# Kernel tuning notes

Hardware: AMD Instinct MI355X
Metric: run time of the kernel (lower is better)

The kernel has to match this reference:

```python
import jax, jax.numpy as jnp
import numpy as np

N, E, F_IN, F_OUT = 50000, 1600000, 256, 64
ALPHA = 0.2  # LeakyReLU negative slope


def setup_inputs() -> dict:
    key = jax.random.key(0)
    k1, k2, k3, k4 = jax.random.split(key, 4)
    x = jax.random.normal(k1, (N, F_IN), dtype=jnp.float32)
    edge = jax.random.randint(k2, (2, E), 0, N)  # COO (row, col) indices of adj
    # xavier_normal with gain=1.414 (as in the torch module)
    W = jax.random.normal(k3, (F_IN, F_OUT), dtype=jnp.float32) * (1.414 * np.sqrt(2.0 / (F_IN + F_OUT)))
    a = jax.random.normal(k4, (1, 2 * F_OUT), dtype=jnp.float32) * (1.414 * np.sqrt(2.0 / (1 + 2 * F_OUT)))
    return {"x": x, "edge": edge, "W": W, "a": a}


def reference(x, edge, W, a):
    # eval mode: dropout is a no-op
    Wh = x @ W  # [N, F_OUT]
    src, dst = edge[0], edge[1]
    # a @ concat(Wh[src], Wh[dst]) per edge, computed as two node-level dots then gathered
    s_src = Wh @ a[0, :F_OUT]   # [N]
    s_dst = Wh @ a[0, F_OUT:]   # [N]
    score = s_src[src] + s_dst[dst]                      # [E]
    edge_e = jnp.exp(-jax.nn.leaky_relu(score, ALPHA))   # [E]
    # sparse-softmax denominator: row sums of exp scores
    e_rowsum = jax.ops.segment_sum(edge_e, src, num_segments=N)  # [N]
    # weighted aggregation: h_prime[i] = sum_{(i,j) in E} e_ij * Wh[j]
    h_prime = jax.ops.segment_sum(edge_e[:, None] * Wh[dst], src, num_segments=N)  # [N, F_OUT]
    h_prime = h_prime / e_rowsum[:, None]
    return jax.nn.elu(h_prime)  # concat=True -> ELU
```

## Files before the change

### kernel.cpp

```cpp
#include <hip/hip_runtime.h>
#include <hip/hip_fp16.h>

#define N_NODES 50000
#define N_EDGES 1600000
#define F_IN 256
#define F_OUT 64
#define ALPHA 0.2f

#define BS 64
#define NBK 782
#define NSUB 8
#define CAP 384
#define EB 4096
#define NBB 391
#define LDS_CAP 4096
#define OF_CAP 16384

typedef __attribute__((ext_vector_type(8))) short bf16x8;
typedef __attribute__((ext_vector_type(4))) float f32x4;

__device__ inline unsigned short f2bf(float f) {
    unsigned int u = __float_as_uint(f);
    return (unsigned short)((u + 0x7FFFu + ((u >> 16) & 1u)) >> 16);
}
__device__ inline float bf2f(unsigned short b) {
    return __uint_as_float(((unsigned int)b) << 16);
}

__device__ inline void fmix_lo(float& a, unsigned int u, float s) {
    asm("v_fma_mix_f32 %0, %1, %2, %0 op_sel:[0,0,0] op_sel_hi:[1,0,0]"
        : "+v"(a) : "v"(u), "v"(s));
}
__device__ inline void fmix_hi(float& a, unsigned int u, float s) {
    asm("v_fma_mix_f32 %0, %1, %2, %0 op_sel:[1,0,0] op_sel_hi:[1,0,0]"
        : "+v"(a) : "v"(u), "v"(s));
}

__global__ __launch_bounds__(256) void gat_wprep(
    const float* __restrict__ W, unsigned short* __restrict__ Wf,
    int* __restrict__ cnt, int* __restrict__ of_cnt)
{
    const int di = blockIdx.x * 256 + threadIdx.x;
    if (di < NSUB * NBK) cnt[di] = 0;
    if (di == 0) of_cnt[0] = 0;
    const int j    = di & 7;
    const int lane = (di >> 3) & 63;
    const int tile = di >> 9;
    const int ks   = tile >> 2;
    const int nt   = tile & 3;
    const int k = ks * 32 + (lane >> 4) * 8 + j;
    const int n = nt * 16 + (lane & 15);
    Wf[di] = f2bf(W[k * F_OUT + n]);
}

__global__ __launch_bounds__(256) void gat_fused(
    const float* __restrict__ x, const unsigned short* __restrict__ Wf,
    const float* __restrict__ a, unsigned short* __restrict__ Whh,
    float* __restrict__ s_src, float* __restrict__ s_dst,
    const int* __restrict__ edge, int* __restrict__ cnt,
    unsigned int* __restrict__ arr, int* __restrict__ of_cnt,
    int2* __restrict__ of_list)
{
    __shared__ __align__(16) unsigned char smem[32768];
    const int t = threadIdx.x;

    if (blockIdx.x < NBK) {
        unsigned short* Wl = (unsigned short*)smem;
        {
            const float4* __restrict__ src = (const float4*)Wf;
            float4* dst = (float4*)Wl;
            #pragma unroll
            for (int i = 0; i < 8; ++i) dst[t + i * 256] = src[t + i * 256];
        }
        __syncthreads();

        const int lane = t & 63;
        const int w    = t >> 6;
        const int q    = lane >> 4;
        const int c16  = lane & 15;
        const bf16x8* __restrict__ Wfrag = (const bf16x8*)Wl;

        float av[4], av2[4];
        #pragma unroll
        for (int nt = 0; nt < 4; ++nt) {
            av[nt]  = a[nt * 16 + c16];
            av2[nt] = a[F_OUT + nt * 16 + c16];
        }

        const int c = blockIdx.x;
        const int node0 = c * 64 + w * 16;
        int row = node0 + c16;
        if (row >= N_NODES) row = N_NODES - 1;
        const float4* __restrict__ xp = (const float4*)(x + (size_t)row * F_IN);

        float4 xv[16];
        #pragma unroll
        for (int ks = 0; ks < 8; ++ks) {
            xv[2 * ks]     = xp[ks * 8 + q * 2];
            xv[2 * ks + 1] = xp[ks * 8 + q * 2 + 1];
        }

        f32x4 acc[4];
        #pragma unroll
        for (int nt = 0; nt < 4; ++nt) acc[nt] = (f32x4){0.f, 0.f, 0.f, 0.f};

        #pragma unroll
        for (int ks = 0; ks < 8; ++ks) {
            float xf[8] = {xv[2*ks].x,   xv[2*ks].y,   xv[2*ks].z,   xv[2*ks].w,
                           xv[2*ks+1].x, xv[2*ks+1].y, xv[2*ks+1].z, xv[2*ks+1].w};
            bf16x8 ah, al;
            #pragma unroll
            for (int j = 0; j < 8; ++j) {
                const unsigned short h = f2bf(xf[j]);
                ah[j] = (short)h;
                al[j] = (short)f2bf(xf[j] - bf2f(h));
            }
            #pragma unroll
            for (int nt = 0; nt < 4; ++nt) {
                const bf16x8 bh = Wfrag[(ks * 4 + nt) * 64 + lane];
                acc[nt] = __builtin_amdgcn_mfma_f32_16x16x32_bf16(ah, bh, acc[nt], 0, 0, 0);
                acc[nt] = __builtin_amdgcn_mfma_f32_16x16x32_bf16(al, bh, acc[nt], 0, 0, 0);
            }
        }

        #pragma unroll
        for (int r = 0; r < 4; ++r) {
            const int node = node0 + q * 4 + r;
            float p = 0.f, qq = 0.f;
            #pragma unroll
            for (int nt = 0; nt < 4; ++nt) {
                const float v = acc[nt][r];
                if (node < N_NODES)
                    Whh[(size_t)node * F_OUT + nt * 16 + c16] =
                        __half_as_ushort(__float2half(v));
                p  = fmaf(v, av[nt], p);
                qq = fmaf(v, av2[nt], qq);
            }
            #pragma unroll
            for (int off = 1; off <= 8; off <<= 1) {
                p  += __shfl_xor(p, off);
                qq += __shfl_xor(qq, off);
            }
            if (c16 == 0 && node < N_NODES) { s_src[node] = p; s_dst[node] = qq; }
        }
    } else {
        int* lhist            = (int*)smem;
        int* lstart           = (int*)(smem + 3128);
        int* gbase            = (int*)(smem + 6260);
        int* cursor           = (int*)(smem + 9388);
        int* scanbuf          = (int*)(smem + 12516);
        unsigned int* sorted  = (unsigned int*)(smem + 13540);

        const int blk = blockIdx.x - NBK;
        const int e0  = blk * EB;
        const int sub = blk & 7;

        for (int i = t; i < NBK; i += 256) lhist[i] = 0;
        __syncthreads();

        int sreg[EB / 256];
        #pragma unroll
        for (int i = 0; i < EB / 256; ++i) {
            const int e = e0 + i * 256 + t;
            int s = -1;
            if (e < N_EDGES) {
                s = edge[e];
                atomicAdd(&lhist[s >> 6], 1);
            }
            sreg[i] = s;
        }
        __syncthreads();

        int psum = 0;
        {
            const int b0 = t * 4;
            #pragma unroll
            for (int i = 0; i < 4; ++i)
                if (b0 + i < NBK) psum += lhist[b0 + i];
        }
        scanbuf[t] = psum;
        __syncthreads();
        for (int off = 1; off < 256; off <<= 1) {
            const int v = (t >= off) ? scanbuf[t - off] : 0;
            __syncthreads();
            scanbuf[t] += v;
            __syncthreads();
        }
        {
            int run = scanbuf[t] - psum;
            const int b0 = t * 4;
            #pragma unroll
            for (int i = 0; i < 4; ++i) {
                const int b = b0 + i;
                if (b < NBK) {
                    lstart[b] = run;
                    cursor[b] = run;
                    run += lhist[b];
                }
            }
            if (t == 255) lstart[NBK] = scanbuf[255];
        }
        __syncthreads();

        for (int b = t; b < NBK; b += 256) {
            const int c = lhist[b];
            gbase[b] = (c > 0) ? atomicAdd(&cnt[sub * NBK + b], c) : 0;
        }

        #pragma unroll
        for (int i = 0; i < EB / 256; ++i) {
            const int s = sreg[i];
            if (s >= 0) {
                const int e = e0 + i * 256 + t;
                const int d = edge[N_EDGES + e];
                const int b = s >> 6;
                const int pos = atomicAdd(&cursor[b], 1);
                sorted[pos] = ((unsigned)b << 22) | ((unsigned)(s & 63) << 16) | (unsigned)d;
            }
        }
        __syncthreads();

        const int C = lstart[NBK];
        for (int p = t; p < C; p += 256) {
            const unsigned en = sorted[p];
            const int b = (int)(en >> 22);
            const int idx = gbase[b] + (p - lstart[b]);
            if (idx < CAP) {
                arr[((size_t)(sub * NBK + b)) * CAP + idx] = en & 0x3FFFFFu;
            } else {
                const int s = b * 64 + (int)((en >> 16) & 63);
                const int op = atomicAdd(of_cnt, 1);
                if (op < OF_CAP) of_list[op] = make_int2(s, (int)(en & 0xFFFFu));
            }
        }
    }
}

__global__ __launch_bounds__(512) void gat_aggregate(
    const int* __restrict__ cnt, const unsigned int* __restrict__ arr,
    const float* __restrict__ s_src, const float* __restrict__ s_dst,
    const unsigned short* __restrict__ Whh, const int* __restrict__ of_cnt,
    const int2* __restrict__ of_list, float* __restrict__ out)
{
    __shared__ uint2 ent2[LDS_CAP + 32];
    __shared__ int   bin[BS];
    __shared__ int   start[BS + 1];
    __shared__ int   Pl[NSUB + 1];
    const int t = threadIdx.x;
    const int lane = t & 63;
    const int w = t >> 6;
    const int b = blockIdx.x;

    if (t < BS) bin[t] = 0;
    if (t < 32) ent2[LDS_CAP + t] = make_uint2(0u, 0u);
    if (w == 0) {
        int c = (lane < NSUB) ? min(cnt[lane * NBK + b], CAP) : 0;
        int s = c;
        #pragma unroll
        for (int off = 1; off < NSUB; off <<= 1) {
            const int v = __shfl_up(s, off);
            if (lane >= off) s += v;
        }
        if (lane < NSUB) Pl[lane + 1] = s;
        if (lane == 0)   Pl[0] = 0;
    }
    __syncthreads();
    const int C = Pl[NSUB];
    const int nof = min(of_cnt[0], OF_CAP);

    unsigned enr[6];
    int nr = 0;
    for (int g = t; g < C; g += 512) {
        int sub = 0;
        #pragma unroll
        for (int s2 = 1; s2 < NSUB; ++s2) sub += (g >= Pl[s2]);
        const unsigned en = arr[((size_t)(sub * NBK + b)) * CAP + (g - Pl[sub])];
        enr[nr++] = en;
        atomicAdd(&bin[en >> 16], 1);
    }
    for (int i = t; i < nof; i += 512) {
        const int2 e2 = of_list[i];
        if ((e2.x >> 6) == b) atomicAdd(&bin[e2.x & 63], 1);
    }
    __syncthreads();
    if (w == 0) {
        const int c  = bin[lane];
        const int pc = (c + 31) & ~31;
        int s = pc;
        #pragma unroll
        for (int off = 1; off < BS; off <<= 1) {
            const int v = __shfl_up(s, off);
            if (lane >= off) s += v;
        }
        start[lane + 1] = s;
        if (lane == 0) start[0] = 0;
        bin[lane] = s - pc;
    }
    __syncthreads();

    for (int r = 0; r < nr; ++r) {
        const unsigned en = enr[r];
        const int sl = (int)(en >> 16);
        const int d  = (int)(en & 0xffffu);
        const float sc = s_src[b * BS + sl] + s_dst[d];
        const float ee = __expf(-(sc > 0.f ? sc : ALPHA * sc));
        const int pos = atomicAdd(&bin[sl], 1);
        if (pos < LDS_CAP) ent2[pos] = make_uint2((unsigned)d, __float_as_uint(ee));
    }
    for (int i = t; i < nof; i += 512) {
        const int2 e2 = of_list[i];
        if ((e2.x >> 6) == b) {
            const float sc = s_src[e2.x] + s_dst[e2.y];
            const float ee = __expf(-(sc > 0.f ? sc : ALPHA * sc));
            const int pos = atomicAdd(&bin[e2.x & 63], 1);
            if (pos < LDS_CAP) ent2[pos] = make_uint2((unsigned)e2.y, __float_as_uint(ee));
        }
    }
    __syncthreads();
    {
        const int n  = t & 63;
        const int e1 = min(start[n + 1], LDS_CAP);
        for (int p = bin[n] + (t >> 6); p < e1; p += 8)
            ent2[p] = make_uint2(0u, 0u);
    }
    __syncthreads();

    const int q  = lane >> 4;
    const int fq = lane & 15;
    const uint2* __restrict__ Whh2 = (const uint2*)Whh;

    for (int n = w * 8; n < w * 8 + 8; ++n) {
        const int node = b * BS + n;
        if (node >= N_NODES) break;
        const int r0 = start[n];
        const int r1 = min(start[n + 1], LDS_CAP);
        float4 acc = make_float4(0.f, 0.f, 0.f, 0.f);
        float rsum = 0.f;
        for (int j = r0; j < r1; j += 32) {
            unsigned eu[8];
            uint2 wv[8];
            #pragma unroll
            for (int k = 0; k < 8; ++k) {
                const uint2 e = ent2[j + 4 * k + q];
                eu[k] = e.y;
                wv[k] = Whh2[(size_t)e.x * 16 + fq];
            }
            #pragma unroll
            for (int k = 0; k < 8; ++k) {
                const float et = __uint_as_float(eu[k]);
                fmix_lo(acc.x, wv[k].x, et);
                fmix_hi(acc.y, wv[k].x, et);
                fmix_lo(acc.z, wv[k].y, et);
                fmix_hi(acc.w, wv[k].y, et);
                rsum += et;
            }
        }
        acc.x += __shfl_xor(acc.x, 16); acc.x += __shfl_xor(acc.x, 32);
        acc.y += __shfl_xor(acc.y, 16); acc.y += __shfl_xor(acc.y, 32);
        acc.z += __shfl_xor(acc.z, 16); acc.z += __shfl_xor(acc.z, 32);
        acc.w += __shfl_xor(acc.w, 16); acc.w += __shfl_xor(acc.w, 32);
        rsum  += __shfl_xor(rsum, 16);  rsum  += __shfl_xor(rsum, 32);

        const float rinv = __builtin_amdgcn_rcpf(rsum);
        float4 v;
        v.x = acc.x * rinv; v.y = acc.y * rinv;
        v.z = acc.z * rinv; v.w = acc.w * rinv;
        v.x = v.x > 0.f ? v.x : (__expf(v.x) - 1.f);
        v.y = v.y > 0.f ? v.y : (__expf(v.y) - 1.f);
        v.z = v.z > 0.f ? v.z : (__expf(v.z) - 1.f);
        v.w = v.w > 0.f ? v.w : (__expf(v.w) - 1.f);
        if (q == 0)
            ((float4*)out)[(size_t)node * 16 + fq] = v;
    }
}

extern "C" void kernel_launch(void* const* d_in, const int* in_sizes, int n_in,
                              void* d_out, int out_size, void* d_ws, size_t ws_size,
                              hipStream_t stream) {
    const float* x    = (const float*)d_in[0];
    const int*   edge = (const int*)  d_in[1];
    const float* W    = (const float*)d_in[2];
    const float* a    = (const float*)d_in[3];
    float* out = (float*)d_out;

    unsigned short* Whh   = (unsigned short*)d_ws;
    unsigned int*   arr   = (unsigned int*)(Whh + (size_t)N_NODES * F_OUT);
    float*          s_src = (float*)(arr + (size_t)NSUB * NBK * CAP);
    float*          s_dst = s_src + N_NODES;
    int*            cnt   = (int*)(s_dst + N_NODES);
    int2*           of_list = (int2*)(cnt + NSUB * NBK);
    int*            of_cnt  = (int*)(of_list + OF_CAP);
    unsigned short* Wf      = (unsigned short*)(of_cnt + 4);

    gat_wprep<<<64, 256, 0, stream>>>(W, Wf, cnt, of_cnt);
    gat_fused<<<NBK + NBB, 256, 0, stream>>>(x, Wf, a, Whh, s_src, s_dst,
                                             edge, cnt, arr, of_cnt, of_list);
    gat_aggregate<<<NBK, 512, 0, stream>>>(cnt, arr, s_src, s_dst, Whh,
                                           of_cnt, of_list, out);
}
```

Measured before the change: 154.7 us.

## Split aggregation into score and gather kernels with packed bf16 CSR

The aggregation kernel is split in two. A score kernel computes edge weights and writes a per-node CSR to global memory, packing the destination index and a bf16 weight into one 32-bit word. A separate gather kernel then assigns one wavefront per node across 6250 blocks, which gives more parallelism and load balance than the old 8 nodes per wave in LDS. The fused kernel's block order is also swapped so the edge-sorting blocks are scheduled first. The trade-offs are an extra global round trip and a kernel launch, plus bf16 rounding of the edge weights.

Result: slower. 159.7 us (+3.2%).

```diff
diff --git a/kernel.cpp b/kernel.cpp
--- a/kernel.cpp
+++ b/kernel.cpp
@@ -13,7 +13,7 @@
 #define CAP 384
 #define EB 4096
 #define NBB 391
-#define LDS_CAP 4096
+#define BCAP 4096
 #define OF_CAP 16384
 
 typedef __attribute__((ext_vector_type(8))) short bf16x8;
@@ -64,7 +64,7 @@
     __shared__ __align__(16) unsigned char smem[32768];
     const int t = threadIdx.x;
 
-    if (blockIdx.x < NBK) {
+    if (blockIdx.x >= NBB) {
         unsigned short* Wl = (unsigned short*)smem;
         {
             const float4* __restrict__ src = (const float4*)Wf;
@@ -87,7 +87,7 @@
             av2[nt] = a[F_OUT + nt * 16 + c16];
         }
 
-        const int c = blockIdx.x;
+        const int c = blockIdx.x - NBB;
         const int node0 = c * 64 + w * 16;
         int row = node0 + c16;
         if (row >= N_NODES) row = N_NODES - 1;
@@ -151,7 +151,7 @@
         int* scanbuf          = (int*)(smem + 12516);
         unsigned int* sorted  = (unsigned int*)(smem + 13540);
 
-        const int blk = blockIdx.x - NBK;
+        const int blk = blockIdx.x;
         const int e0  = blk * EB;
         const int sub = blk & 7;
 
@@ -236,23 +236,22 @@
     }
 }
 
-__global__ __launch_bounds__(512) void gat_aggregate(
+__global__ __launch_bounds__(512) void gat_score(
     const int* __restrict__ cnt, const unsigned int* __restrict__ arr,
     const float* __restrict__ s_src, const float* __restrict__ s_dst,
-    const unsigned short* __restrict__ Whh, const int* __restrict__ of_cnt,
-    const int2* __restrict__ of_list, float* __restrict__ out)
+    const int* __restrict__ of_cnt, const int2* __restrict__ of_list,
+    unsigned int* __restrict__ csr, int* __restrict__ abase,
+    int* __restrict__ pcnt)
 {
-    __shared__ uint2 ent2[LDS_CAP + 32];
-    __shared__ int   bin[BS];
-    __shared__ int   start[BS + 1];
-    __shared__ int   Pl[NSUB + 1];
+    __shared__ int bin[BS];
+    __shared__ int start[BS + 1];
+    __shared__ int Pl[NSUB + 1];
     const int t = threadIdx.x;
     const int lane = t & 63;
     const int w = t >> 6;
     const int b = blockIdx.x;
 
     if (t < BS) bin[t] = 0;
-    if (t < 32) ent2[LDS_CAP + t] = make_uint2(0u, 0u);
     if (w == 0) {
         int c = (lane < NSUB) ? min(cnt[lane * NBK + b], CAP) : 0;
         int s = c;
@@ -297,6 +296,8 @@
         bin[lane] = s - pc;
     }
     __syncthreads();
+
+    unsigned int* __restrict__ csrb = csr + (size_t)b * BCAP;
 
     for (int r = 0; r < nr; ++r) {
         const unsigned en = enr[r];
@@ -305,7 +306,7 @@
         const float sc = s_src[b * BS + sl] + s_dst[d];
         const float ee = __expf(-(sc > 0.f ? sc : ALPHA * sc));
         const int pos = atomicAdd(&bin[sl], 1);
-        if (pos < LDS_CAP) ent2[pos] = make_uint2((unsigned)d, __float_as_uint(ee));
+        if (pos < BCAP) csrb[pos] = ((unsigned)d << 16) | (unsigned)f2bf(ee);
     }
     for (int i = t; i < nof; i += 512) {
         const int2 e2 = of_list[i];
@@ -313,65 +314,75 @@
             const float sc = s_src[e2.x] + s_dst[e2.y];
             const float ee = __expf(-(sc > 0.f ? sc : ALPHA * sc));
             const int pos = atomicAdd(&bin[e2.x & 63], 1);
-            if (pos < LDS_CAP) ent2[pos] = make_uint2((unsigned)e2.y, __float_as_uint(ee));
+            if (pos < BCAP) csrb[pos] = ((unsigned)e2.y << 16) | (unsigned)f2bf(ee);
         }
     }
     __syncthreads();
     {
         const int n  = t & 63;
-        const int e1 = min(start[n + 1], LDS_CAP);
-        for (int p = bin[n] + (t >> 6); p < e1; p += 8)
-            ent2[p] = make_uint2(0u, 0u);
-    }
-    __syncthreads();
-
+        const int e1 = min(start[n + 1], BCAP);
+        for (int p = bin[n] + (t >> 6); p < e1; p += 8) csrb[p] = 0u;
+    }
+    if (t < BS) {
+        const int s0 = min(start[t], BCAP);
+        abase[b * BS + t] = b * BCAP + s0;
+        pcnt[b * BS + t]  = min(start[t + 1], BCAP) - s0;
+    }
+}
+
+__global__ __launch_bounds__(512) void gat_gather(
+    const int* __restrict__ abase, const int* __restrict__ pcnt,
+    const unsigned int* __restrict__ csr,
+    const unsigned short* __restrict__ Whh, float* __restrict__ out)
+{
+    const int t = threadIdx.x;
+    const int lane = t & 63;
+    const int w = t >> 6;
+    const int node = blockIdx.x * 8 + w;
     const int q  = lane >> 4;
     const int fq = lane & 15;
+
+    const int base = abase[node];
+    const int cn   = pcnt[node];
     const uint2* __restrict__ Whh2 = (const uint2*)Whh;
 
-    for (int n = w * 8; n < w * 8 + 8; ++n) {
-        const int node = b * BS + n;
-        if (node >= N_NODES) break;
-        const int r0 = start[n];
-        const int r1 = min(start[n + 1], LDS_CAP);
-        float4 acc = make_float4(0.f, 0.f, 0.f, 0.f);
-        float rsum = 0.f;
-        for (int j = r0; j < r1; j += 32) {
-            unsigned eu[8];
-            uint2 wv[8];
-            #pragma unroll
-            for (int k = 0; k < 8; ++k) {
-                const uint2 e = ent2[j + 4 * k + q];
-                eu[k] = e.y;
-                wv[k] = Whh2[(size_t)e.x * 16 + fq];
-            }
-            #pragma unroll
-            for (int k = 0; k < 8; ++k) {
-                const float et = __uint_as_float(eu[k]);
-                fmix_lo(acc.x, wv[k].x, et);
-                fmix_hi(acc.y, wv[k].x, et);
-                fmix_lo(acc.z, wv[k].y, et);
-                fmix_hi(acc.w, wv[k].y, et);
-                rsum += et;
-            }
-        }
-        acc.x += __shfl_xor(acc.x, 16); acc.x += __shfl_xor(acc.x, 32);
-        acc.y += __shfl_xor(acc.y, 16); acc.y += __shfl_xor(acc.y, 32);
-        acc.z += __shfl_xor(acc.z, 16); acc.z += __shfl_xor(acc.z, 32);
-        acc.w += __shfl_xor(acc.w, 16); acc.w += __shfl_xor(acc.w, 32);
-        rsum  += __shfl_xor(rsum, 16);  rsum  += __shfl_xor(rsum, 32);
-
-        const float rinv = __builtin_amdgcn_rcpf(rsum);
-        float4 v;
-        v.x = acc.x * rinv; v.y = acc.y * rinv;
-        v.z = acc.z * rinv; v.w = acc.w * rinv;
-        v.x = v.x > 0.f ? v.x : (__expf(v.x) - 1.f);
-        v.y = v.y > 0.f ? v.y : (__expf(v.y) - 1.f);
-        v.z = v.z > 0.f ? v.z : (__expf(v.z) - 1.f);
-        v.w = v.w > 0.f ? v.w : (__expf(v.w) - 1.f);
-        if (q == 0)
-            ((float4*)out)[(size_t)node * 16 + fq] = v;
-    }
+    float4 acc = make_float4(0.f, 0.f, 0.f, 0.f);
+    float rsum = 0.f;
+    for (int j = 0; j < cn; j += 32) {
+        const uint4* __restrict__ cp = (const uint4*)(csr + base + j);
+        const uint4 wa = cp[q * 2];
+        const uint4 wb = cp[q * 2 + 1];
+        const unsigned wd[8] = {wa.x, wa.y, wa.z, wa.w, wb.x, wb.y, wb.z, wb.w};
+        uint2 wv[8];
+        #pragma unroll
+        for (int k = 0; k < 8; ++k)
+            wv[k] = Whh2[(size_t)(wd[k] >> 16) * 16 + fq];
+        #pragma unroll
+        for (int k = 0; k < 8; ++k) {
+            const float et = __uint_as_float(wd[k] << 16);
+            fmix_lo(acc.x, wv[k].x, et);
+            fmix_hi(acc.y, wv[k].x, et);
+            fmix_lo(acc.z, wv[k].y, et);
+            fmix_hi(acc.w, wv[k].y, et);
+            rsum += et;
+        }
+    }
+    acc.x += __shfl_xor(acc.x, 16); acc.x += __shfl_xor(acc.x, 32);
+    acc.y += __shfl_xor(acc.y, 16); acc.y += __shfl_xor(acc.y, 32);
+    acc.z += __shfl_xor(acc.z, 16); acc.z += __shfl_xor(acc.z, 32);
+    acc.w += __shfl_xor(acc.w, 16); acc.w += __shfl_xor(acc.w, 32);
+    rsum  += __shfl_xor(rsum, 16);  rsum  += __shfl_xor(rsum, 32);
+
+    const float rinv = __builtin_amdgcn_rcpf(rsum);
+    float4 v;
+    v.x = acc.x * rinv; v.y = acc.y * rinv;
+    v.z = acc.z * rinv; v.w = acc.w * rinv;
+    v.x = v.x > 0.f ? v.x : (__expf(v.x) - 1.f);
+    v.y = v.y > 0.f ? v.y : (__expf(v.y) - 1.f);
+    v.z = v.z > 0.f ? v.z : (__expf(v.z) - 1.f);
+    v.w = v.w > 0.f ? v.w : (__expf(v.w) - 1.f);
+    if (q == 0)
+        ((float4*)out)[(size_t)node * 16 + fq] = v;
 }
 
 extern "C" void kernel_launch(void* const* d_in, const int* in_sizes, int n_in,
@@ -384,17 +395,21 @@
     float* out = (float*)d_out;
 
     unsigned short* Whh   = (unsigned short*)d_ws;
-    unsigned int*   arr   = (unsigned int*)(Whh + (size_t)N_NODES * F_OUT);
+    unsigned int*   csr   = (unsigned int*)(Whh + (size_t)N_NODES * F_OUT);
+    unsigned int*   arr   = csr + (size_t)NBK * BCAP;
     float*          s_src = (float*)(arr + (size_t)NSUB * NBK * CAP);
     float*          s_dst = s_src + N_NODES;
     int*            cnt   = (int*)(s_dst + N_NODES);
-    int2*           of_list = (int2*)(cnt + NSUB * NBK);
+    int*            abase = cnt + NSUB * NBK;
+    int*            pcnt  = abase + NBK * BS;
+    int2*           of_list = (int2*)(pcnt + NBK * BS);
     int*            of_cnt  = (int*)(of_list + OF_CAP);
     unsigned short* Wf      = (unsigned short*)(of_cnt + 4);
 
     gat_wprep<<<64, 256, 0, stream>>>(W, Wf, cnt, of_cnt);
     gat_fused<<<NBK + NBB, 256, 0, stream>>>(x, Wf, a, Whh, s_src, s_dst,
                                              edge, cnt, arr, of_cnt, of_list);
-    gat_aggregate<<<NBK, 512, 0, stream>>>(cnt, arr, s_src, s_dst, Whh,
-                                           of_cnt, of_list, out);
-}
+    gat_score<<<NBK, 512, 0, stream>>>(cnt, arr, s_src, s_dst,
+                                       of_cnt, of_list, csr, abase, pcnt);
+    gat_gather<<<6250, 512, 0, stream>>>(abase, pcnt, csr, Whh, out);
+}
```
